# Optimization experiments

Hardware: AMD Instinct MI355X
Metric: run time of the kernel (lower is better)

Reference implementation:

```python
import jax, jax.numpy as jnp
import numpy as np

M, H = 7, 200                 # ensemble size, hidden width
OBS, ACT = 32, 8
C = OBS + ACT                 # model input dim
DOUT = OBS + 1                # next-obs delta + reward
N = 100000                    # number of transitions
E_NUM = 5                     # number of elites
MAX_LOGVAR, MIN_LOGVAR = 0.5, -10.0
REWARD_SCALE, REWARD_BIAS = 1.0, 0.0
TERM_THRESH = 50.0


def setup_inputs() -> dict:
    key = jax.random.key(0)
    ks = jax.random.split(key, 10)
    def w(k, shape, fan_in):
        return jax.random.normal(k, shape, jnp.float32) / np.float32(np.sqrt(fan_in))
    return {
        "observations": jax.random.normal(ks[0], (N, OBS), jnp.float32),
        "actions": jax.random.normal(ks[1], (N, ACT), jnp.float32),
        "scaler_mu": jax.random.normal(ks[2], (C,), jnp.float32) * 0.1,
        "scaler_std": jax.random.uniform(ks[3], (C,), jnp.float32, 0.5, 1.5),
        "W1": w(ks[4], (M, C, H), C), "b1": jnp.zeros((M, 1, H), jnp.float32),
        "W2": w(ks[5], (M, H, H), H), "b2": jnp.zeros((M, 1, H), jnp.float32),
        "W3": w(ks[6], (M, H, H), H), "b3": jnp.zeros((M, 1, H), jnp.float32),
        "W4": w(ks[7], (M, H, 2 * DOUT), H), "b4": jnp.zeros((M, 1, 2 * DOUT), jnp.float32),
        "elites": jnp.arange(E_NUM, dtype=jnp.int32),
    }


def _ensemble_mlp(z, W1, b1, W2, b2, W3, b3, W4, b4):
    # z: [M, R, C] -> mean, logvar: [M, R, DOUT]
    h = jax.nn.swish(jnp.einsum('mrc,mch->mrh', z, W1) + b1)
    h = jax.nn.swish(jnp.einsum('mrh,mhk->mrk', h, W2) + b2)
    h = jax.nn.swish(jnp.einsum('mrh,mhk->mrk', h, W3) + b3)
    out = jnp.einsum('mrh,mhk->mrk', h, W4) + b4
    mean, logvar = out[..., :DOUT], out[..., DOUT:]
    logvar = MAX_LOGVAR - jax.nn.softplus(MAX_LOGVAR - logvar)
    logvar = MIN_LOGVAR + jax.nn.softplus(logvar - MIN_LOGVAR)
    return mean, logvar


def _terminal_fn(observations, actions, next_obs):
    # simple environment-style terminal predicate, shape [N, 1]
    return jnp.linalg.norm(next_obs, axis=-1, keepdims=True) > TERM_THRESH


def reference(observations, actions, scaler_mu, scaler_std,
              W1, b1, W2, b2, W3, b3, W4, b4, elites):
    key = jax.random.key(0)  # source uses the SAME key for permutation and noise
    z = jnp.concatenate([observations, actions], axis=1)
    z = (z - scaler_mu) / scaler_std
    n, c = z.shape
    e = elites.shape[0]
    r = (n - 1) // e + 1
    pad = e * r - n
    z = jnp.concatenate([z, jnp.zeros((pad, c), z.dtype)], axis=0)
    idxs = jax.random.permutation(key, e * r)
    tmp = z[idxs].reshape(e, r, c)                    # dispatch to elite slots
    zf = jnp.zeros((M, r, c), z.dtype).at[elites].set(tmp)
    mean, logvar = _ensemble_mlp(zf, W1, b1, W2, b2, W3, b3, W4, b4)
    std = jnp.exp(0.5 * logvar)
    ensemble_samples = mean + jax.random.normal(key, mean.shape) * std
    res = ensemble_samples[elites].reshape(e * r, DOUT)   # gather elites back
    es = jnp.zeros((e * r, DOUT), res.dtype).at[idxs].set(res)[:n]  # inverse perm
    samples = jnp.concatenate([es[:, :-1] + observations, es[:, -1:]], axis=1)
    next_obs = samples[..., :-1]
    reward = samples[..., -1] * REWARD_SCALE + REWARD_BIAS
    terminal = _terminal_fn(observations, actions, next_obs).squeeze(1)
    return next_obs, reward, terminal
```

## Files before the change

### kernel.cpp

```cpp
#include <hip/hip_runtime.h>
#include <stdint.h>

#define N_TOT   100000
#define NPAD    100352
#define NBLK    98
#define HISTN   (256 * NBLK)
#define R_PER   20000
#define NOISE_HALF 2310000u
#define PERM_HALF  50000u

#define JAX_PARTITIONABLE 1

#define ROWS 32
#define RG_N 2
#define BPM  625
#define MLP_GRID (5 * BPM)
#define KST  208

#define L1_U4 1664
#define L2_U4 5824
#define L4_U4 2240
#define PM_U4 (L1_U4 + 2 * L2_U4 + L4_U4)
#define L1OFF 0
#define L2OFF L1_U4
#define L3OFF (L1_U4 + L2_U4)
#define L4OFF (L1_U4 + 2 * L2_U4)
#define WPACK_BLOCKS 304

using f32x4  = __attribute__((ext_vector_type(4))) float;
using bf16x8 = __attribute__((ext_vector_type(8))) short;

__host__ __device__ __forceinline__ uint32_t rotl32(uint32_t x, unsigned d) {
  return (x << d) | (x >> (32u - d));
}

__host__ __device__ inline void tf2x32(uint32_t k0, uint32_t k1,
                                       uint32_t x0, uint32_t x1,
                                       uint32_t& o0, uint32_t& o1) {
  uint32_t k2 = k0 ^ k1 ^ 0x1BD11BDAu;
  x0 += k0; x1 += k1;
#define TFR(R) { x0 += x1; x1 = rotl32(x1, R); x1 ^= x0; }
  TFR(13u) TFR(15u) TFR(26u) TFR(6u)
  x0 += k1; x1 += k2 + 1u;
  TFR(17u) TFR(29u) TFR(16u) TFR(24u)
  x0 += k2; x1 += k0 + 2u;
  TFR(13u) TFR(15u) TFR(26u) TFR(6u)
  x0 += k0; x1 += k1 + 3u;
  TFR(17u) TFR(29u) TFR(16u) TFR(24u)
  x0 += k1; x1 += k2 + 4u;
  TFR(13u) TFR(15u) TFR(26u) TFR(6u)
  x0 += k2; x1 += k0 + 5u;
#undef TFR
  o0 = x0; o1 = x1;
}

__host__ __device__ inline uint32_t jax_bits32(uint32_t k0, uint32_t k1,
                                               uint32_t idx, uint32_t half) {
#if JAX_PARTITIONABLE
  (void)half;
  uint32_t o0, o1; tf2x32(k0, k1, 0u, idx, o0, o1);
  return o0 ^ o1;
#else
  uint32_t o0, o1;
  if (idx < half) { tf2x32(k0, k1, idx, idx + half, o0, o1); return o0; }
  else            { tf2x32(k0, k1, idx - half, idx, o0, o1); return o1; }
#endif
}

static void jax_split_host(uint32_t k0, uint32_t k1,
                           uint32_t* nk, uint32_t* sk) {
#if JAX_PARTITIONABLE
  tf2x32(k0, k1, 0u, 0u, nk[0], nk[1]);
  tf2x32(k0, k1, 0u, 1u, sk[0], sk[1]);
#else
  uint32_t a0, a1, b0, b1;
  tf2x32(k0, k1, 0u, 2u, a0, a1);
  tf2x32(k0, k1, 1u, 3u, b0, b1);
  nk[0] = a0; nk[1] = b0;
  sk[0] = a1; sk[1] = b1;
#endif
}

__device__ __forceinline__ void split2(float e0, float e1,
                                       uint32_t& hi, uint32_t& lo) {
  uint32_t u0 = __float_as_uint(e0), u1 = __float_as_uint(e1);
  float f0 = __uint_as_float(u0 & 0xFFFF0000u);
  float f1 = __uint_as_float(u1 & 0xFFFF0000u);
  uint32_t l0 = __float_as_uint(e0 - f0) >> 16;
  uint32_t l1 = __float_as_uint(e1 - f1) >> 16;
  hi = (u1 & 0xFFFF0000u) | (u0 >> 16);
  lo = (l1 << 16) | l0;
}

__device__ __forceinline__ void split1(float x, unsigned short& h,
                                       unsigned short& l) {
  uint32_t u = __float_as_uint(x);
  float fh = __uint_as_float(u & 0xFFFF0000u);
  h = (unsigned short)(u >> 16);
  l = (unsigned short)(__float_as_uint(x - fh) >> 16);
}

__device__ __forceinline__ float rec1(unsigned short h, unsigned short l) {
  return __uint_as_float((uint32_t)h << 16) + __uint_as_float((uint32_t)l << 16);
}

__device__ __forceinline__ bf16x8 punu4(uint4 x) {
  union { uint4 u; bf16x8 v; } t;
  t.u = x;
  return t.v;
}

__global__ __launch_bounds__(256) void k_pre(uint32_t kk0, uint32_t kk1,
                                             uint32_t* __restrict__ keys,
                                             uint32_t* __restrict__ vals,
                                             uint32_t* __restrict__ hist,
                                             uint32_t* __restrict__ histZ,
                                             const float* __restrict__ W1,
                                             const float* __restrict__ W2,
                                             const float* __restrict__ W3,
                                             const float* __restrict__ W4,
                                             uint4* __restrict__ wpH,
                                             uint4* __restrict__ wpL) {
  __shared__ uint32_t h[256];
  int tid = threadIdx.x;
  if (blockIdx.x < NBLK) {
    int b = blockIdx.x;
    h[tid] = 0;
    __syncthreads();
    uint32_t base = b * 1024u + tid * 4u;
    uint32_t kq[4], vq[4];
#pragma unroll
    for (int j = 0; j < 4; ++j) {
      uint32_t i = base + j;
      if (i < (uint32_t)N_TOT) {
        kq[j] = jax_bits32(kk0, kk1, i, PERM_HALF);
        vq[j] = i;
      } else {
        kq[j] = 0xFFFFFFFFu;
        vq[j] = 0xFFFFFFFFu;
      }
      atomicAdd(&h[kq[j] & 255u], 1u);
    }
    *(uint4*)(keys + base) = make_uint4(kq[0], kq[1], kq[2], kq[3]);
    *(uint4*)(vals + base) = make_uint4(vq[0], vq[1], vq[2], vq[3]);
    __syncthreads();
    hist[tid * NBLK + b] = h[tid];
    histZ[tid * NBLK + b] = 0;
  } else {
    int flat = (blockIdx.x - NBLK) * 256 + tid;
    if (flat >= 5 * PM_U4) return;
    int m = flat / PM_U4;
    int rem = flat - m * PM_U4;
    const float* W; int KIN, KOUT, nch, loc;
    if (rem < L2OFF)      { W = W1 + (size_t)m * 40 * 200;  KIN = 40;  KOUT = 200; nch = 2; loc = rem; }
    else if (rem < L3OFF) { W = W2 + (size_t)m * 200 * 200; KIN = 200; KOUT = 200; nch = 7; loc = rem - L2OFF; }
    else if (rem < L4OFF) { W = W3 + (size_t)m * 200 * 200; KIN = 200; KOUT = 200; nch = 7; loc = rem - L3OFF; }
    else                  { W = W4 + (size_t)m * 200 * 66;  KIN = 200; KOUT = 66;  nch = 7; loc = rem - L4OFF; }
    int lane = loc & 63;
    int tc = loc >> 6;
    int ch = tc % nch;
    int t  = tc / nch;
    int g = lane >> 4, cr = lane & 15;
    int k0 = ch * 32 + g * 8;
    int col = t * 16 + cr;
    const bool ok = (k0 < KIN) && (col < KOUT);
    float w[8];
#pragma unroll
    for (int j = 0; j < 8; ++j)
      w[j] = ok ? W[(size_t)(k0 + j) * KOUT + col] : 0.f;
    uint32_t hi[4], lo[4];
#pragma unroll
    for (int d = 0; d < 4; ++d)
      split2(w[2 * d], w[2 * d + 1], hi[d], lo[d]);
    wpH[flat] = make_uint4(hi[0], hi[1], hi[2], hi[3]);
    wpL[flat] = make_uint4(lo[0], lo[1], lo[2], lo[3]);
  }
}

template<bool GENNEXT, bool LAST>
__global__ __launch_bounds__(256) void k_scat(const uint32_t* __restrict__ keyIn,
                                              const uint32_t* __restrict__ valIn,
                                              uint32_t* __restrict__ keyOut,
                                              uint32_t* __restrict__ valOut,
                                              const uint32_t* __restrict__ histRaw,
                                              uint32_t* __restrict__ histNext,
                                              uint32_t* __restrict__ histZero,
                                              int shift, uint32_t nk0, uint32_t nk1) {
  __shared__ __align__(16) uint8_t blob[HISTN * 4];
  __shared__ uint32_t tot[256];
  __shared__ uint32_t bas[256];
  __shared__ uint32_t offD[256];
  int b = blockIdx.x, tid = threadIdx.x;

  uint32_t base = b * 1024u + tid * 4u;
  uint4 kk4 = *(const uint4*)(keyIn + base);
  uint4 vv4 = *(const uint4*)(valIn + base);
  uint32_t k[4] = {kk4.x, kk4.y, kk4.z, kk4.w};
  uint32_t v[4] = {vv4.x, vv4.y, vv4.z, vv4.w};

  {
    uint32_t* ldsH = (uint32_t*)blob;
    for (int x = tid; x < HISTN; x += 256) ldsH[x] = histRaw[x];
    __syncthreads();
    uint32_t before = 0, t = 0;
    for (int b2 = 0; b2 < NBLK; ++b2) {
      uint32_t val = ldsH[tid * NBLK + b2];
      before += (b2 < b) ? val : 0u;
      t += val;
    }
    tot[tid] = t;
    __syncthreads();
    if (tid == 0) {
      uint32_t run = 0;
      for (int i = 0; i < 256; ++i) { bas[i] = run; run += tot[i]; }
    }
    __syncthreads();
    offD[tid] = bas[tid] + before;
    __syncthreads();
  }

  uint32_t* dig   = (uint32_t*)blob;
  uint32_t* histc = (uint32_t*)(blob + 4096);
  uint32_t d[4];
  int cp = tid >> 4;
  for (int x = tid; x < 16 * 256; x += 256) histc[x] = 0;
  __syncthreads();
#pragma unroll
  for (int j = 0; j < 4; ++j) {
    d[j] = (k[j] >> shift) & 255u;
    dig[tid * 4 + j] = d[j];
    atomicAdd(&histc[cp * 256 + d[j]], 1u);
  }
  __syncthreads();
  {
    uint32_t run = 0;
#pragma unroll
    for (int c = 0; c < 16; ++c) {
      uint32_t t = histc[c * 256 + tid];
      histc[c * 256 + tid] = run;
      run += t;
    }
  }
  __syncthreads();
  int c[4] = {0, 0, 0, 0};
  int start = cp * 64;
  int P = tid * 4;
  for (int p = start; p < P; ++p) {
    uint32_t dd = dig[p];
#pragma unroll
    for (int j = 0; j < 4; ++j) c[j] += (dd == d[j]);
  }
  c[1] += (d[0] == d[1]);
  c[2] += (d[0] == d[2]) + (d[1] == d[2]);
  c[3] += (d[0] == d[3]) + (d[1] == d[3]) + (d[2] == d[3]);
#pragma unroll
  for (int j = 0; j < 4; ++j) {
    uint32_t rank = histc[cp * 256 + d[j]] + (uint32_t)c[j];
    uint32_t off = offD[d[j]] + rank;
    valOut[off] = v[j];
    if (!LAST) {
      uint32_t nkey;
      int nshift;
      if (GENNEXT) {
        nkey = (off < (uint32_t)N_TOT) ? jax_bits32(nk0, nk1, off, PERM_HALF)
                                       : 0xFFFFFFFFu;
        nshift = 0;
      } else {
        nkey = k[j];
        nshift = shift + 8;
      }
      keyOut[off] = nkey;
      atomicAdd(&histNext[((nkey >> nshift) & 255u) * NBLK + (off >> 10)], 1u);
    }
  }
  if (!LAST) histZero[b * 256 + tid] = 0;
}

__device__ inline float softplusf(float x) {
  float ax = fabsf(x);
  float r = log1pf(expf(-ax));
  return (x > 0.f) ? x + r : r;
}

__device__ inline float erfinvf_approx(float x) {
  float w = -logf((1.0f - x) * (1.0f + x));
  float p;
  if (w < 5.0f) {
    w = w - 2.5f;
    p = 2.81022636e-08f;
    p = fmaf(p, w, 3.43273939e-07f);
    p = fmaf(p, w, -3.5233877e-06f);
    p = fmaf(p, w, -4.39150654e-06f);
    p = fmaf(p, w, 0.00021858087f);
    p = fmaf(p, w, -0.00125372503f);
    p = fmaf(p, w, -0.00417768164f);
    p = fmaf(p, w, 0.246640727f);
    p = fmaf(p, w, 1.50140941f);
  } else {
    w = sqrtf(w) - 3.0f;
    p = -0.000200214257f;
    p = fmaf(p, w, 0.000100950558f);
    p = fmaf(p, w, 0.00134934322f);
    p = fmaf(p, w, -0.00367342844f);
    p = fmaf(p, w, 0.00573950773f);
    p = fmaf(p, w, -0.0076224613f);
    p = fmaf(p, w, 0.00943887047f);
    p = fmaf(p, w, 1.00167406f);
    p = fmaf(p, w, 2.83297682f);
  }
  return p * x;
}

template<int KOUT, int NTILES, int NCH, bool ACTV>
__device__ __forceinline__ void layer_mfma(unsigned short* __restrict__ Ahi,
                                           unsigned short* __restrict__ Alo,
                                           const uint4* __restrict__ wpH,
                                           const uint4* __restrict__ wpL,
                                           int woff,
                                           const float* __restrict__ bm,
                                           int wv, int lane) {
  constexpr int MAXT = (NTILES + 3) / 4;
  const int g  = lane >> 4;
  const int cr = lane & 15;
  f32x4 acc[RG_N][MAXT];
#pragma unroll
  for (int rg = 0; rg < RG_N; ++rg)
#pragma unroll
    for (int ti = 0; ti < MAXT; ++ti)
      acc[rg][ti] = (f32x4){0.f, 0.f, 0.f, 0.f};

  for (int ch = 0; ch < NCH; ++ch) {
    const int k0 = ch * 32 + g * 8;
    const bool ok = (k0 + 8 <= KST);
    const int ka = ok ? k0 : 0;
    uint4 hfa[RG_N], lfa[RG_N];
#pragma unroll
    for (int rg = 0; rg < RG_N; ++rg) {
      uint4 h = *(const uint4*)(Ahi + (rg * 16 + cr) * KST + ka);
      uint4 l = *(const uint4*)(Alo + (rg * 16 + cr) * KST + ka);
      if (!ok) { h = make_uint4(0, 0, 0, 0); l = make_uint4(0, 0, 0, 0); }
      hfa[rg] = h; lfa[rg] = l;
    }
#pragma unroll
    for (int ti = 0; ti < MAXT; ++ti) {
      const int t = wv + ti * 4;
      if (t < NTILES) {
        const int idx = woff + (t * NCH + ch) * 64 + lane;
        bf16x8 vbh = punu4(wpH[idx]);
        bf16x8 vbl = punu4(wpL[idx]);
#pragma unroll
        for (int rg = 0; rg < RG_N; ++rg) {
          bf16x8 vah = punu4(hfa[rg]);
          bf16x8 val = punu4(lfa[rg]);
          acc[rg][ti] = __builtin_amdgcn_mfma_f32_16x16x32_bf16(vah, vbh, acc[rg][ti], 0, 0, 0);
          acc[rg][ti] = __builtin_amdgcn_mfma_f32_16x16x32_bf16(val, vbh, acc[rg][ti], 0, 0, 0);
          acc[rg][ti] = __builtin_amdgcn_mfma_f32_16x16x32_bf16(vah, vbl, acc[rg][ti], 0, 0, 0);
        }
      }
    }
  }
  __syncthreads();
#pragma unroll
  for (int ti = 0; ti < MAXT; ++ti) {
    const int t = wv + ti * 4;
    if (t < NTILES) {
      const int col = t * 16 + cr;
      if (col < KOUT) {
        const float bias = bm[col];
#pragma unroll
        for (int rg = 0; rg < RG_N; ++rg) {
#pragma unroll
          for (int rr = 0; rr < 4; ++rr) {
            float x = acc[rg][ti][rr] + bias;
            if (ACTV) x = x / (1.0f + expf(-x));
            unsigned short h, l;
            split1(x, h, l);
            const int row = rg * 16 + g * 4 + rr;
            Ahi[row * KST + col] = h;
            Alo[row * KST + col] = l;
          }
        }
      }
    }
  }
  __syncthreads();
}

__global__ __launch_bounds__(256, 5) void k_mlp(
    const float* __restrict__ obs, const float* __restrict__ act,
    const float* __restrict__ mu, const float* __restrict__ sst,
    const uint4* __restrict__ wpH, const uint4* __restrict__ wpL,
    const float* __restrict__ b1, const float* __restrict__ b2,
    const float* __restrict__ b3, const float* __restrict__ b4,
    const uint32_t* __restrict__ idxs, float* __restrict__ outv) {
  __shared__ __align__(16) unsigned short Ahi[ROWS * KST];
  __shared__ __align__(16) unsigned short Alo[ROWS * KST];
  __shared__ uint32_t jrow[ROWS];
  __shared__ float nrm[ROWS];
  __shared__ float muv[40];
  __shared__ float rsd[40];
  const int tid = threadIdx.x;
  const int m  = blockIdx.x / BPM;
  const int bb = blockIdx.x - m * BPM;
  const int i0 = m * R_PER + bb * ROWS;
  const int wv = tid >> 6;
  const int lane = tid & 63;
  const int mw = m * PM_U4;

  if (tid < ROWS) {
    jrow[tid] = idxs[i0 + tid];
    nrm[tid] = 0.f;
  }
  if (tid >= 64 && tid < 104) {
    int cc = tid - 64;
    muv[cc] = mu[cc];
    rsd[cc] = 1.0f / sst[cc];
  }
  __syncthreads();

  for (int t = tid; t < ROWS * 64; t += 256) {
    int rr = t >> 6, cc = t & 63;
    float v = 0.f;
    if (cc < 40) {
      uint32_t j = jrow[rr];
      float x = (cc < 32) ? obs[(size_t)j * 32 + cc] : act[(size_t)j * 8 + (cc - 32)];
      v = (x - muv[cc]) * rsd[cc];
    }
    unsigned short h, l;
    split1(v, h, l);
    Ahi[rr * KST + cc] = h;
    Alo[rr * KST + cc] = l;
  }
  for (int t = tid; t < ROWS * 8; t += 256) {
    int rr = t >> 3, cc = 200 + (t & 7);
    Ahi[rr * KST + cc] = 0;
    Alo[rr * KST + cc] = 0;
  }
  __syncthreads();

  layer_mfma<200, 13, 2, true >(Ahi, Alo, wpH, wpL, mw + L1OFF, b1 + (size_t)m * 200, wv, lane);
  layer_mfma<200, 13, 7, true >(Ahi, Alo, wpH, wpL, mw + L2OFF, b2 + (size_t)m * 200, wv, lane);
  layer_mfma<200, 13, 7, true >(Ahi, Alo, wpH, wpL, mw + L3OFF, b3 + (size_t)m * 200, wv, lane);
  layer_mfma< 66,  5, 7, false>(Ahi, Alo, wpH, wpL, mw + L4OFF, b4 + (size_t)m * 66, wv, lane);

  float* onext = outv;
  float* orew  = outv + 3200000;
  float* oterm = outv + 3300000;

  for (int t = tid; t < ROWS * 33; t += 256) {
    int rw = t / 33, kc = t - rw * 33;
    float mean = rec1(Ahi[rw * KST + kc],      Alo[rw * KST + kc]);
    float lvr  = rec1(Ahi[rw * KST + 33 + kc], Alo[rw * KST + 33 + kc]);
    float lv = 0.5f - softplusf(0.5f - lvr);
    lv = -10.0f + softplusf(lv + 10.0f);
    float sd = expf(0.5f * lv);
    int q = bb * ROWS + rw;
    uint32_t tno = (uint32_t)(m * 660000 + q * 33 + kc);
    uint32_t bits = jax_bits32(0u, 0u, tno, NOISE_HALF);
    float f = __uint_as_float((bits >> 9) | 0x3F800000u) - 1.0f;
    const float LOu = -0.99999994f;
    float u = fmaxf(LOu, fmaf(f, 2.0f, LOu));
    float nz = 1.41421356237f * erfinvf_approx(u);
    float s = mean + nz * sd;
    uint32_t j = jrow[rw];
    if (kc < 32) {
      float no = s + obs[(size_t)j * 32 + kc];
      onext[(size_t)j * 32 + kc] = no;
      atomicAdd(&nrm[rw], no * no);
    } else {
      orew[j] = s;
    }
  }
  __syncthreads();
  if (tid < ROWS) {
    uint32_t j = jrow[tid];
    oterm[j] = (sqrtf(nrm[tid]) > 50.0f) ? 1.0f : 0.0f;
  }
}

extern "C" void kernel_launch(void* const* d_in, const int* in_sizes, int n_in,
                              void* d_out, int out_size, void* d_ws, size_t ws_size,
                              hipStream_t stream) {
  (void)in_sizes; (void)n_in; (void)out_size; (void)ws_size;
  const float* obs = (const float*)d_in[0];
  const float* act = (const float*)d_in[1];
  const float* mu  = (const float*)d_in[2];
  const float* sst = (const float*)d_in[3];
  const float* W1  = (const float*)d_in[4];
  const float* b1  = (const float*)d_in[5];
  const float* W2  = (const float*)d_in[6];
  const float* b2  = (const float*)d_in[7];
  const float* W3  = (const float*)d_in[8];
  const float* b3  = (const float*)d_in[9];
  const float* W4  = (const float*)d_in[10];
  const float* b4  = (const float*)d_in[11];

  uint8_t* ws = (uint8_t*)d_ws;
  uint32_t* keysA = (uint32_t*)(ws);
  uint32_t* keysB = (uint32_t*)(ws + 401408);
  uint32_t* valsA = (uint32_t*)(ws + 802816);
  uint32_t* valsB = (uint32_t*)(ws + 1204224);
  uint32_t* hA    = (uint32_t*)(ws + 1605632);
  uint32_t* hB    = (uint32_t*)(ws + 1705984);
  uint32_t* hC    = (uint32_t*)(ws + 1806336);
  uint4*    wpH   = (uint4*)(ws + 1906688);
  uint4*    wpL   = (uint4*)(ws + 3150848);

  uint32_t key0[2] = {0u, 0u}, key1[2], sub1[2], key2[2], sub2[2];
  jax_split_host(key0[0], key0[1], key1, sub1);
  jax_split_host(key1[0], key1[1], key2, sub2);

  dim3 g(NBLK), blk(256);

  k_pre<<<dim3(NBLK + WPACK_BLOCKS), blk, 0, stream>>>(sub1[0], sub1[1],
      keysA, valsA, hA, hB, W1, W2, W3, W4, wpH, wpL);
  k_scat<false,false><<<g, blk, 0, stream>>>(keysA, valsA, keysB, valsB, hA, hB, hC, 0,  0u, 0u);
  k_scat<false,false><<<g, blk, 0, stream>>>(keysB, valsB, keysA, valsA, hB, hC, hA, 8,  0u, 0u);
  k_scat<false,false><<<g, blk, 0, stream>>>(keysA, valsA, keysB, valsB, hC, hA, hB, 16, 0u, 0u);
  k_scat<true, false><<<g, blk, 0, stream>>>(keysB, valsB, keysA, valsA, hA, hB, hC, 24, sub2[0], sub2[1]);
  k_scat<false,false><<<g, blk, 0, stream>>>(keysA, valsA, keysB, valsB, hB, hC, hA, 0,  0u, 0u);
  k_scat<false,false><<<g, blk, 0, stream>>>(keysB, valsB, keysA, valsA, hC, hA, hB, 8,  0u, 0u);
  k_scat<false,false><<<g, blk, 0, stream>>>(keysA, valsA, keysB, valsB, hA, hB, hC, 16, 0u, 0u);
  k_scat<false,true ><<<g, blk, 0, stream>>>(keysB, valsB, keysA, valsA, hB, hC, hA, 24, 0u, 0u);

  k_mlp<<<dim3(MLP_GRID), blk, 0, stream>>>(obs, act, mu, sst,
                                            wpH, wpL, b1, b2, b3, b4,
                                            valsA, (float*)d_out);
}
```

Before: 356.3 us.

## Use 1024-thread radix scatter blocks with parallel scan; shrink MLP LDS stride

The radix-sort scatter kernel now runs 1024 threads per block, one key per thread instead of four, and replaces the serial single-thread prefix over 256 digits with a Hillis-Steele parallel scan. The MLP kernel's activation row stride drops from 208 to 200 shorts and the padding zero-fill is removed. Its launch-bounds occupancy hint rises from 5 to 6 blocks. Together these aim to cut serial work in the eight scatter passes and lower LDS and register pressure in the MLP. The tighter stride may raise LDS bank conflicts, and dropping the padding could leave stale data if any loads read columns 200-207.

```diff
diff --git a/kernel.cpp b/kernel.cpp
--- a/kernel.cpp
+++ b/kernel.cpp
@@ -15,7 +15,7 @@
 #define RG_N 2
 #define BPM  625
 #define MLP_GRID (5 * BPM)
-#define KST  208
+#define KST  200
 
 #define L1_U4 1664
 #define L2_U4 5824
@@ -178,61 +178,59 @@
 }
 
 template<bool GENNEXT, bool LAST>
-__global__ __launch_bounds__(256) void k_scat(const uint32_t* __restrict__ keyIn,
-                                              const uint32_t* __restrict__ valIn,
-                                              uint32_t* __restrict__ keyOut,
-                                              uint32_t* __restrict__ valOut,
-                                              const uint32_t* __restrict__ histRaw,
-                                              uint32_t* __restrict__ histNext,
-                                              uint32_t* __restrict__ histZero,
-                                              int shift, uint32_t nk0, uint32_t nk1) {
+__global__ __launch_bounds__(1024) void k_scat(const uint32_t* __restrict__ keyIn,
+                                               const uint32_t* __restrict__ valIn,
+                                               uint32_t* __restrict__ keyOut,
+                                               uint32_t* __restrict__ valOut,
+                                               const uint32_t* __restrict__ histRaw,
+                                               uint32_t* __restrict__ histNext,
+                                               uint32_t* __restrict__ histZero,
+                                               int shift, uint32_t nk0, uint32_t nk1) {
   __shared__ __align__(16) uint8_t blob[HISTN * 4];
   __shared__ uint32_t tot[256];
   __shared__ uint32_t bas[256];
+  __shared__ uint32_t bef[256];
   __shared__ uint32_t offD[256];
-  int b = blockIdx.x, tid = threadIdx.x;
-
-  uint32_t base = b * 1024u + tid * 4u;
-  uint4 kk4 = *(const uint4*)(keyIn + base);
-  uint4 vv4 = *(const uint4*)(valIn + base);
-  uint32_t k[4] = {kk4.x, kk4.y, kk4.z, kk4.w};
-  uint32_t v[4] = {vv4.x, vv4.y, vv4.z, vv4.w};
+  const int b = blockIdx.x, tid = threadIdx.x;
+
+  const uint32_t key = keyIn[b * 1024 + tid];
+  const uint32_t val = valIn[b * 1024 + tid];
 
   {
     uint32_t* ldsH = (uint32_t*)blob;
-    for (int x = tid; x < HISTN; x += 256) ldsH[x] = histRaw[x];
+    for (int x = tid; x < HISTN; x += 1024) ldsH[x] = histRaw[x];
     __syncthreads();
-    uint32_t before = 0, t = 0;
-    for (int b2 = 0; b2 < NBLK; ++b2) {
-      uint32_t val = ldsH[tid * NBLK + b2];
-      before += (b2 < b) ? val : 0u;
-      t += val;
-    }
-    tot[tid] = t;
+    if (tid < 256) {
+      uint32_t before = 0, t = 0;
+      for (int b2 = 0; b2 < NBLK; ++b2) {
+        uint32_t v2 = ldsH[tid * NBLK + b2];
+        before += (b2 < b) ? v2 : 0u;
+        t += v2;
+      }
+      tot[tid] = t; bef[tid] = before; bas[tid] = t;
+    }
     __syncthreads();
-    if (tid == 0) {
-      uint32_t run = 0;
-      for (int i = 0; i < 256; ++i) { bas[i] = run; run += tot[i]; }
-    }
-    __syncthreads();
-    offD[tid] = bas[tid] + before;
+    for (int off = 1; off < 256; off <<= 1) {
+      uint32_t v = 0;
+      if (tid < 256 && tid >= off) v = bas[tid - off];
+      __syncthreads();
+      if (tid < 256) bas[tid] += v;
+      __syncthreads();
+    }
+    if (tid < 256) offD[tid] = bas[tid] - tot[tid] + bef[tid];
     __syncthreads();
   }
 
   uint32_t* dig   = (uint32_t*)blob;
   uint32_t* histc = (uint32_t*)(blob + 4096);
-  uint32_t d[4];
-  int cp = tid >> 4;
-  for (int x = tid; x < 16 * 256; x += 256) histc[x] = 0;
-  __syncthreads();
-#pragma unroll
-  for (int j = 0; j < 4; ++j) {
-    d[j] = (k[j] >> shift) & 255u;
-    dig[tid * 4 + j] = d[j];
-    atomicAdd(&histc[cp * 256 + d[j]], 1u);
-  }
-  __syncthreads();
-  {
+  const uint32_t d = (key >> shift) & 255u;
+  const int cp = tid >> 6;
+  for (int x = tid; x < 16 * 256; x += 1024) histc[x] = 0;
+  __syncthreads();
+  dig[tid] = d;
+  atomicAdd(&histc[cp * 256 + d], 1u);
+  __syncthreads();
+  if (tid < 256) {
     uint32_t run = 0;
 #pragma unroll
     for (int c = 0; c < 16; ++c) {
@@ -242,38 +240,27 @@
     }
   }
   __syncthreads();
-  int c[4] = {0, 0, 0, 0};
-  int start = cp * 64;
-  int P = tid * 4;
-  for (int p = start; p < P; ++p) {
-    uint32_t dd = dig[p];
-#pragma unroll
-    for (int j = 0; j < 4; ++j) c[j] += (dd == d[j]);
-  }
-  c[1] += (d[0] == d[1]);
-  c[2] += (d[0] == d[2]) + (d[1] == d[2]);
-  c[3] += (d[0] == d[3]) + (d[1] == d[3]) + (d[2] == d[3]);
-#pragma unroll
-  for (int j = 0; j < 4; ++j) {
-    uint32_t rank = histc[cp * 256 + d[j]] + (uint32_t)c[j];
-    uint32_t off = offD[d[j]] + rank;
-    valOut[off] = v[j];
-    if (!LAST) {
-      uint32_t nkey;
-      int nshift;
-      if (GENNEXT) {
-        nkey = (off < (uint32_t)N_TOT) ? jax_bits32(nk0, nk1, off, PERM_HALF)
-                                       : 0xFFFFFFFFu;
-        nshift = 0;
-      } else {
-        nkey = k[j];
-        nshift = shift + 8;
-      }
-      keyOut[off] = nkey;
-      atomicAdd(&histNext[((nkey >> nshift) & 255u) * NBLK + (off >> 10)], 1u);
-    }
-  }
-  if (!LAST) histZero[b * 256 + tid] = 0;
+  int c = 0;
+  for (int p = cp * 64; p < tid; ++p)
+    c += (dig[p] == d);
+  const uint32_t rank = histc[cp * 256 + d] + (uint32_t)c;
+  const uint32_t off = offD[d] + rank;
+  valOut[off] = val;
+  if (!LAST) {
+    uint32_t nkey;
+    int nshift;
+    if (GENNEXT) {
+      nkey = (off < (uint32_t)N_TOT) ? jax_bits32(nk0, nk1, off, PERM_HALF)
+                                     : 0xFFFFFFFFu;
+      nshift = 0;
+    } else {
+      nkey = key;
+      nshift = shift + 8;
+    }
+    keyOut[off] = nkey;
+    atomicAdd(&histNext[((nkey >> nshift) & 255u) * NBLK + (off >> 10)], 1u);
+    if (tid < 256) histZero[b * 256 + tid] = 0;
+  }
 }
 
 __device__ inline float softplusf(float x) {
@@ -386,7 +373,7 @@
   __syncthreads();
 }
 
-__global__ __launch_bounds__(256, 5) void k_mlp(
+__global__ __launch_bounds__(256, 6) void k_mlp(
     const float* __restrict__ obs, const float* __restrict__ act,
     const float* __restrict__ mu, const float* __restrict__ sst,
     const uint4* __restrict__ wpH, const uint4* __restrict__ wpL,
@@ -430,11 +417,6 @@
     split1(v, h, l);
     Ahi[rr * KST + cc] = h;
     Alo[rr * KST + cc] = l;
-  }
-  for (int t = tid; t < ROWS * 8; t += 256) {
-    int rr = t >> 3, cc = 200 + (t & 7);
-    Ahi[rr * KST + cc] = 0;
-    Alo[rr * KST + cc] = 0;
   }
   __syncthreads();
 
@@ -510,18 +492,18 @@
   jax_split_host(key0[0], key0[1], key1, sub1);
   jax_split_host(key1[0], key1[1], key2, sub2);
 
-  dim3 g(NBLK), blk(256);
+  dim3 g(NBLK), blk(256), blk1k(1024);
 
   k_pre<<<dim3(NBLK + WPACK_BLOCKS), blk, 0, stream>>>(sub1[0], sub1[1],
       keysA, valsA, hA, hB, W1, W2, W3, W4, wpH, wpL);
-  k_scat<false,false><<<g, blk, 0, stream>>>(keysA, valsA, keysB, valsB, hA, hB, hC, 0,  0u, 0u);
-  k_scat<false,false><<<g, blk, 0, stream>>>(keysB, valsB, keysA, valsA, hB, hC, hA, 8,  0u, 0u);
-  k_scat<false,false><<<g, blk, 0, stream>>>(keysA, valsA, keysB, valsB, hC, hA, hB, 16, 0u, 0u);
-  k_scat<true, false><<<g, blk, 0, stream>>>(keysB, valsB, keysA, valsA, hA, hB, hC, 24, sub2[0], sub2[1]);
-  k_scat<false,false><<<g, blk, 0, stream>>>(keysA, valsA, keysB, valsB, hB, hC, hA, 0,  0u, 0u);
-  k_scat<false,false><<<g, blk, 0, stream>>>(keysB, valsB, keysA, valsA, hC, hA, hB, 8,  0u, 0u);
-  k_scat<false,false><<<g, blk, 0, stream>>>(keysA, valsA, keysB, valsB, hA, hB, hC, 16, 0u, 0u);
-  k_scat<false,true ><<<g, blk, 0, stream>>>(keysB, valsB, keysA, valsA, hB, hC, hA, 24, 0u, 0u);
+  k_scat<false,false><<<g, blk1k, 0, stream>>>(keysA, valsA, keysB, valsB, hA, hB, hC, 0,  0u, 0u);
+  k_scat<false,false><<<g, blk1k, 0, stream>>>(keysB, valsB, keysA, valsA, hB, hC, hA, 8,  0u, 0u);
+  k_scat<false,false><<<g, blk1k, 0, stream>>>(keysA, valsA, keysB, valsB, hC, hA, hB, 16, 0u, 0u);
+  k_scat<true, false><<<g, blk1k, 0, stream>>>(keysB, valsB, keysA, valsA, hA, hB, hC, 24, sub2[0], sub2[1]);
+  k_scat<false,false><<<g, blk1k, 0, stream>>>(keysA, valsA, keysB, valsB, hB, hC, hA, 0,  0u, 0u);
+  k_scat<false,false><<<g, blk1k, 0, stream>>>(keysB, valsB, keysA, valsA, hC, hA, hB, 8,  0u, 0u);
+  k_scat<false,false><<<g, blk1k, 0, stream>>>(keysA, valsA, keysB, valsB, hA, hB, hC, 16, 0u, 0u);
+  k_scat<false,true ><<<g, blk1k, 0, stream>>>(keysB, valsB, keysA, valsA, hB, hC, hA, 24, 0u, 0u);
 
   k_mlp<<<dim3(MLP_GRID), blk, 0, stream>>>(obs, act, mu, sst,
                                             wpH, wpL, b1, b2, b3, b4,
```

New measurement: 307.3 us (median of 2 runs). -13.8%, faster.
